# Performance work log

Hardware: AMD Instinct MI355X
Metric: run time of the kernel (lower is better)

The kernel has to match this reference:

```python
import jax, jax.numpy as jnp
import numpy as np

N = 100000   # total nodes in batched graph
E = 320000   # total edges
B = 128      # number of graphs in batch
D_IN = 128
H = 256
OUT = 10
L = 4        # num_layers - 1 conv layers
EPS = 1e-6


def setup_inputs() -> dict:
    key = jax.random.key(0)
    ks = jax.random.split(key, 8)
    h = jax.random.normal(ks[0], (N, D_IN), dtype=jnp.float32)
    src = jax.random.randint(ks[1], (E,), 0, N)
    dst = jax.random.randint(ks[2], (E,), 0, N)
    batch_ids = jnp.sort(jax.random.randint(ks[3], (N,), 0, B))
    s = 0.05
    W_first = jax.random.normal(ks[4], (D_IN, H), dtype=jnp.float32) * s
    b_first = jnp.zeros((H,), jnp.float32)
    W_rest = jax.random.normal(ks[5], (L - 1, H, H), dtype=jnp.float32) * s
    b_rest = jnp.zeros((L - 1, H), jnp.float32)
    gamma = jnp.ones((L, H), jnp.float32)
    beta = jnp.zeros((L, H), jnp.float32)
    mean_scale = jnp.ones((L, H), jnp.float32)
    W_pred = jax.random.normal(ks[6], (H, OUT), dtype=jnp.float32) * s
    b_pred = jnp.zeros((OUT,), jnp.float32)
    return dict(h=h, src=src, dst=dst, batch_ids=batch_ids,
                W_first=W_first, b_first=b_first, W_rest=W_rest, b_rest=b_rest,
                gamma=gamma, beta=beta, mean_scale=mean_scale,
                W_pred=W_pred, b_pred=b_pred)


def _graph_conv(h, W, b, src, dst, dinv_src, dinv_dst):
    # DGL GraphConv, norm='both': D_dst^{-1/2} A D_src^{-1/2} h W + b
    x = h * dinv_src[:, None]
    m = jax.ops.segment_sum(x[src], dst, num_segments=N)
    m = m * dinv_dst[:, None]
    return m @ W + b


def _graph_norm(h, gamma, beta, ms, batch_ids, counts):
    # GraphNorm: per-graph mean (scaled by learnable mean_scale) and std
    mean = jax.ops.segment_sum(h, batch_ids, num_segments=B) / counts[:, None]
    sub = h - mean[batch_ids] * ms
    var = jax.ops.segment_sum(sub * sub, batch_ids, num_segments=B) / counts[:, None]
    inv_std = jax.lax.rsqrt(var + EPS)
    return gamma * sub * inv_std[batch_ids] + beta


def reference(h, src, dst, batch_ids, W_first, b_first, W_rest, b_rest,
              gamma, beta, mean_scale, W_pred, b_pred):
    ones_e = jnp.ones((E,), h.dtype)
    deg_out = jnp.maximum(jax.ops.segment_sum(ones_e, src, num_segments=N), 1.0)
    deg_in = jnp.maximum(jax.ops.segment_sum(ones_e, dst, num_segments=N), 1.0)
    dinv_src = jax.lax.rsqrt(deg_out)
    dinv_dst = jax.lax.rsqrt(deg_in)
    counts = jnp.maximum(
        jax.ops.segment_sum(jnp.ones((N,), h.dtype), batch_ids, num_segments=B), 1.0)

    for i in range(L):
        x = h
        if i == 0:
            h = _graph_conv(h, W_first, b_first, src, dst, dinv_src, dinv_dst)
        else:
            h = _graph_conv(h, W_rest[i - 1], b_rest[i - 1], src, dst, dinv_src, dinv_dst)
        h = _graph_norm(h, gamma[i], beta[i], mean_scale[i], batch_ids, counts)
        if i != 0:
            h = jax.nn.relu(h) + x
        else:
            h = jax.nn.relu(h)

    pooled = jax.ops.segment_sum(h, batch_ids, num_segments=B)  # [B, H]
    # dropout is identity at eval
    return pooled @ W_pred + b_pred
```

## Files before the change

### kernel.cpp

```cpp
#include <hip/hip_runtime.h>

#define N_NODES 100000
#define N_PAD   100096
#define N_EDGES 320000
#define NB      128
#define DIN     128
#define H       256
#define OUT_DIM 10
#define EPSV    1e-6f
#define SCAN_B  256
#define PSLICES 32
#define NBLK    (N_PAD / 64)
#define NXCD    8
#define GEMM_PGRID 1024

typedef unsigned short bf16_t;
typedef __attribute__((ext_vector_type(8))) short bf16x8;
typedef __attribute__((ext_vector_type(4))) float f32x4;

__device__ __forceinline__ float bf2f(bf16_t u) {
    union { unsigned int i; float f; } x;
    x.i = ((unsigned int)u) << 16;
    return x.f;
}
__device__ __forceinline__ bf16_t f2bf(float f) {
    union { float f; unsigned int i; } x;
    x.f = f;
    unsigned int r = x.i + 0x7fffu + ((x.i >> 16) & 1u);
    return (bf16_t)(r >> 16);
}

__device__ __forceinline__ int xcd_swz(int bid, int nwg) {
    int q = nwg / NXCD, r = nwg % NXCD;
    int x = bid % NXCD, j = bid / NXCD;
    int base = (x < r) ? x * (q + 1) : r * (q + 1) + (x - r) * q;
    return base + j;
}

__global__ void k_edge_deg(const int* __restrict__ src, const int* __restrict__ dst,
                           int* deg_out, int* deg_in) {
    int e = blockIdx.x * blockDim.x + threadIdx.x;
    if (e < N_EDGES) {
        atomicAdd(&deg_out[src[e]], 1);
        atomicAdd(&deg_in[dst[e]], 1);
    }
}

__global__ void k_dinv(const int* __restrict__ deg_out, const int* __restrict__ deg_in,
                       float* dinv_src, float* dinv_dst) {
    int n = blockIdx.x * blockDim.x + threadIdx.x;
    if (n < N_NODES) {
        dinv_src[n] = rsqrtf((float)max(deg_out[n], 1));
        dinv_dst[n] = rsqrtf((float)max(deg_in[n], 1));
    }
}

__global__ void k_gstart(const int* __restrict__ bid, int* __restrict__ gstart,
                         float* __restrict__ countsf) {
    int b = threadIdx.x;
    if (b <= NB) {
        int lo = 0, hi = N_NODES;
        while (lo < hi) {
            int mid = (lo + hi) >> 1;
            if (bid[mid] < b) lo = mid + 1; else hi = mid;
        }
        gstart[b] = lo;
    }
    __syncthreads();
    if (b < NB) countsf[b] = (float)max(gstart[b + 1] - gstart[b], 1);
}

__global__ void k_relpk(const int* __restrict__ bid, unsigned int* __restrict__ relpk) {
    int idx = blockIdx.x * blockDim.x + threadIdx.x;
    if (idx >= NBLK * 16) return;
    int t = idx >> 4, w = idx & 15;
    int row0 = t * 64;
    int g0 = bid[(row0 < N_NODES) ? row0 : (N_NODES - 1)];
    unsigned int pk = 0;
    for (int j = 0; j < 4; ++j) {
        int r = row0 + w * 4 + j;
        unsigned int rel = 255u;
        if (r < N_NODES) {
            int d = bid[r] - g0;
            rel = (d >= 0 && d < 255) ? (unsigned int)d : 255u;
        }
        pk |= rel << (8 * j);
    }
    relpk[idx] = pk;
}

__global__ void k_scan1(const int* __restrict__ deg, int* incl, int* bsums) {
    __shared__ int s[SCAN_B];
    int i = blockIdx.x * SCAN_B + threadIdx.x;
    int v = (i < N_NODES) ? deg[i] : 0;
    s[threadIdx.x] = v;
    __syncthreads();
    for (int d = 1; d < SCAN_B; d <<= 1) {
        int t = (threadIdx.x >= d) ? s[threadIdx.x - d] : 0;
        __syncthreads();
        s[threadIdx.x] += t;
        __syncthreads();
    }
    if (i < N_NODES) incl[i] = s[threadIdx.x];
    if (threadIdx.x == SCAN_B - 1) bsums[blockIdx.x] = s[threadIdx.x];
}

__global__ void k_scan2(const int* __restrict__ bsums, int* boffs, int nb) {
    __shared__ int s[512];
    int t = threadIdx.x;
    int v = (t < nb) ? bsums[t] : 0;
    s[t] = v;
    __syncthreads();
    for (int d = 1; d < 512; d <<= 1) {
        int x = (t >= d) ? s[t - d] : 0;
        __syncthreads();
        s[t] += x;
        __syncthreads();
    }
    if (t < nb) boffs[t] = s[t] - v;
}

__global__ void k_scan3(const int* __restrict__ deg, const int* __restrict__ incl,
                        const int* __restrict__ boffs, int* row_start, int* cursor) {
    int i = blockIdx.x * blockDim.x + threadIdx.x;
    if (i < N_NODES) {
        int ex = incl[i] - deg[i] + boffs[i / SCAN_B];
        row_start[i] = ex;
        cursor[i]    = ex;
    }
    if (i == 0) row_start[N_NODES] = N_EDGES;
}

__global__ void k_scatter(const int* __restrict__ src, const int* __restrict__ dst,
                          int* cursor, int* csr_src) {
    int e = blockIdx.x * blockDim.x + threadIdx.x;
    if (e < N_EDGES) {
        int slot = atomicAdd(&cursor[dst[e]], 1);
        csr_src[slot] = src[e];
    }
}

__global__ void k_wt_first(const float* __restrict__ W, bf16_t* __restrict__ Wt) {
    int idx = blockIdx.x * 256 + threadIdx.x;
    if (idx >= H * DIN) return;
    int c = idx / DIN, k = idx % DIN;
    Wt[idx] = f2bf(W[k * H + c]);
}
__global__ void k_wt_rest(const float* __restrict__ W, bf16_t* __restrict__ Wt) {
    int idx = blockIdx.x * 256 + threadIdx.x;
    if (idx >= 3 * H * H) return;
    int l = idx / (H * H);
    int rem = idx % (H * H);
    int c = rem / H, k = rem % H;
    Wt[idx] = f2bf(W[(size_t)l * H * H + k * H + c]);
}

__global__ void k_prescale(const float* __restrict__ h, const float* __restrict__ dinv_s,
                           bf16_t* __restrict__ hs) {
    int idx = xcd_swz(blockIdx.x, 12500) * 256 + threadIdx.x;
    if (idx >= N_NODES * (DIN / 4)) return;
    int n = idx >> 5;
    float w = dinv_s[n];
    float4 v = reinterpret_cast<const float4*>(h)[idx];
    ushort4 o;
    o.x = f2bf(v.x * w); o.y = f2bf(v.y * w);
    o.z = f2bf(v.z * w); o.w = f2bf(v.w * w);
    reinterpret_cast<ushort4*>(hs)[idx] = o;
}

template <int NC, bool PS>
__global__ void k_agg(const bf16_t* __restrict__ hx, const float* __restrict__ dinv_s,
                      const float* __restrict__ dinv_d, const int* __restrict__ row_start,
                      const int* __restrict__ csr_src, bf16_t* __restrict__ m) {
    constexpr int VEC = NC / 64;
    int gid  = xcd_swz(blockIdx.x, 25000) * blockDim.x + threadIdx.x;
    int v    = gid >> 6;
    int lane = gid & 63;
    if (v >= N_NODES) return;
    float acc[VEC] = {};
    int s0 = row_start[v], s1 = row_start[v + 1];

    auto body = [&](int ei) {
        int si = csr_src[ei];
        float wv = 1.f;
        if constexpr (!PS) wv = dinv_s[si];
        if constexpr (VEC == 4) {
            ushort4 r = *reinterpret_cast<const ushort4*>(hx + (size_t)si * NC + lane * 4);
            acc[0] += bf2f(r.x) * wv; acc[1] += bf2f(r.y) * wv;
            acc[2] += bf2f(r.z) * wv; acc[3] += bf2f(r.w) * wv;
        } else {
            ushort2 r = *reinterpret_cast<const ushort2*>(hx + (size_t)si * NC + lane * 2);
            acc[0] += bf2f(r.x) * wv; acc[1] += bf2f(r.y) * wv;
        }
    };

    int e = s0;
    for (; e + 3 < s1; e += 4) { body(e); body(e + 1); body(e + 2); body(e + 3); }
    for (; e < s1; ++e) body(e);

    float wd = dinv_d[v];
    if constexpr (VEC == 4) {
        ushort4 o;
        o.x = f2bf(acc[0] * wd); o.y = f2bf(acc[1] * wd);
        o.z = f2bf(acc[2] * wd); o.w = f2bf(acc[3] * wd);
        *reinterpret_cast<ushort4*>(m + (size_t)v * NC + lane * 4) = o;
    } else {
        ushort2 o; o.x = f2bf(acc[0] * wd); o.y = f2bf(acc[1] * wd);
        *reinterpret_cast<ushort2*>(m + (size_t)v * NC + lane * 2) = o;
    }
}

template <int K>
__global__ __launch_bounds__(256, 2) void k_gemm_mfma(const bf16_t* __restrict__ A,
                                                      const bf16_t* __restrict__ Wt,
                                                      const float* __restrict__ bias,
                                                      const unsigned int* __restrict__ relpk,
                                                      bf16_t* __restrict__ C,
                                                      float2* __restrict__ part) {
    __shared__ bf16_t lds_raw[64 * (H + 8)];
    constexpr int LKA = K + 8;
    bf16_t (*aT)[LKA] = reinterpret_cast<bf16_t (*)[LKA]>(lds_raw);
    bf16_t (*cT)[H + 8] = reinterpret_cast<bf16_t (*)[H + 8]>(lds_raw);
    constexpr int KS = K / 32;

    const int tid  = threadIdx.x;
    const int wave = tid >> 6;
    const int lane = tid & 63;
    const int col0 = wave * 64;
    const int lr = lane & 15;
    const int lg = lane >> 4;

    const bf16_t* Bb = Wt + (size_t)(col0 + lr) * K + lg * 8;
    bf16x8 ball[KS][4];
    #pragma unroll
    for (int ks = 0; ks < KS; ++ks)
        #pragma unroll
        for (int nt = 0; nt < 4; ++nt)
            ball[ks][nt] = *reinterpret_cast<const bf16x8*>(Bb + (size_t)nt * 16 * K + ks * 32);
    float bsn[4];
    #pragma unroll
    for (int nt = 0; nt < 4; ++nt) bsn[nt] = bias[col0 + nt * 16 + lr];

    for (int t = blockIdx.x; t < NBLK; t += GEMM_PGRID) {
        const int pb   = xcd_swz(t, NBLK);
        const int row0 = pb * 64;

        {
            const bf16_t* Ag = A + (size_t)row0 * K;
            constexpr int CHUNKS = 64 * K / 8;
            #pragma unroll
            for (int it = 0; it < CHUNKS / 256; ++it) {
                int ci  = it * 256 + tid;
                int row = (ci * 8) / K;
                int col = (ci * 8) % K;
                uint4 v = *reinterpret_cast<const uint4*>(Ag + ci * 8);
                *reinterpret_cast<uint4*>(&aT[row][col]) = v;
            }
        }
        __syncthreads();

        f32x4 acc[4][4] = {};

        #pragma unroll
        for (int ks = 0; ks < KS; ++ks) {
            bf16x8 a[4];
            #pragma unroll
            for (int mt = 0; mt < 4; ++mt)
                a[mt] = *reinterpret_cast<const bf16x8*>(&aT[mt * 16 + lr][ks * 32 + lg * 8]);
            #pragma unroll
            for (int mt = 0; mt < 4; ++mt)
                #pragma unroll
                for (int nt = 0; nt < 4; ++nt)
                    acc[mt][nt] = __builtin_amdgcn_mfma_f32_16x16x32_bf16(a[mt], ball[ks][nt], acc[mt][nt], 0, 0, 0);
        }

        {
            unsigned int relw[4];
            #pragma unroll
            for (int mt = 0; mt < 4; ++mt)
                relw[mt] = relpk[pb * 16 + mt * 4 + lg];

            float sA[3][4] = {}, qA[3][4] = {};
            #pragma unroll
            for (int mt = 0; mt < 4; ++mt) {
                #pragma unroll
                for (int j = 0; j < 4; ++j) {
                    int rv = (relw[mt] >> (8 * j)) & 0xff;
                    #pragma unroll
                    for (int nt = 0; nt < 4; ++nt) {
                        float v  = acc[mt][nt][j] + bsn[nt];
                        float v0 = (rv == 0) ? v : 0.f;
                        float v1 = (rv == 1) ? v : 0.f;
                        float v2 = (rv == 2) ? v : 0.f;
                        sA[0][nt] += v0; qA[0][nt] += v0 * v0;
                        sA[1][nt] += v1; qA[1][nt] += v1 * v1;
                        sA[2][nt] += v2; qA[2][nt] += v2 * v2;
                    }
                }
            }
            #pragma unroll
            for (int rel = 0; rel < 3; ++rel) {
                #pragma unroll
                for (int nt = 0; nt < 4; ++nt) {
                    float sv = sA[rel][nt], qv = qA[rel][nt];
                    sv += __shfl_xor(sv, 16); qv += __shfl_xor(qv, 16);
                    sv += __shfl_xor(sv, 32); qv += __shfl_xor(qv, 32);
                    sA[rel][nt] = sv; qA[rel][nt] = qv;
                }
            }
            if (lg == 0) {
                constexpr size_t PLANE = (size_t)NBLK * H;
                #pragma unroll
                for (int rel = 0; rel < 3; ++rel)
                    #pragma unroll
                    for (int nt = 0; nt < 4; ++nt)
                        part[(size_t)rel * PLANE + (size_t)pb * H + col0 + nt * 16 + lr]
                            = make_float2(sA[rel][nt], qA[rel][nt]);
            }
        }

        __syncthreads();

        #pragma unroll
        for (int nt = 0; nt < 4; ++nt) {
            int c = col0 + nt * 16 + lr;
            #pragma unroll
            for (int mt = 0; mt < 4; ++mt) {
                #pragma unroll
                for (int j = 0; j < 4; ++j)
                    cT[mt * 16 + lg * 4 + j][c] = f2bf(acc[mt][nt][j] + bsn[nt]);
            }
        }
        __syncthreads();

        #pragma unroll
        for (int it = 0; it < 8; ++it) {
            int i = it * 256 + tid;
            int r = i >> 5;
            int s = i & 31;
            *reinterpret_cast<uint4*>(C + (size_t)(row0 + r) * H + s * 8) =
                *reinterpret_cast<const uint4*>(&cT[r][s * 8]);
        }
        __syncthreads();
    }
}

__global__ void k_stats_red(const float2* __restrict__ part, const int* __restrict__ bid,
                            const int* __restrict__ gstart, const float* __restrict__ countsf,
                            const float* __restrict__ gamma, const float* __restrict__ beta,
                            const float* __restrict__ msc,
                            float* __restrict__ scale, float* __restrict__ shift) {
    constexpr size_t PLANE = (size_t)NBLK * H;
    int b = blockIdx.x;
    int c = threadIdx.x;
    int n0 = gstart[b], n1 = gstart[b + 1];
    float s = 0.f, q = 0.f;
    if (n1 > n0) {
        int blo = n0 >> 6, bhi = (n1 - 1) >> 6;
        for (int blk = blo; blk <= bhi; ++blk) {
            int rel = b - bid[blk << 6];
            if (rel >= 0 && rel < 3) {
                float2 v = part[(size_t)rel * PLANE + (size_t)blk * H + c];
                s += v.x; q += v.y;
            }
        }
    }
    float rc   = 1.0f / countsf[b];
    float mean = s * rc, ex2 = q * rc;
    float mm   = mean * msc[c];
    float var  = ex2 - 2.f * mean * mm + mm * mm;
    float a    = gamma[c] * rsqrtf(var + EPSV);
    scale[b * H + c] = a;
    shift[b * H + c] = beta[c] - a * mm;
}

template <bool RES>
__global__ void k_norm(const bf16_t* __restrict__ y, const bf16_t* __restrict__ resid,
                       const int* __restrict__ bid, const float* __restrict__ scale,
                       const float* __restrict__ shift, bf16_t* __restrict__ outp) {
    int idx = xcd_swz(blockIdx.x, 25000) * 256 + threadIdx.x;
    if (idx >= N_NODES * (H / 4)) return;
    int n  = idx >> 6;
    int f4 = idx & 63;
    int b  = bid[n];
    float4 sc = reinterpret_cast<const float4*>(scale)[b * 64 + f4];
    float4 sh = reinterpret_cast<const float4*>(shift)[b * 64 + f4];
    ushort4 yv = reinterpret_cast<const ushort4*>(y)[idx];
    float o0 = fmaxf(bf2f(yv.x) * sc.x + sh.x, 0.f);
    float o1 = fmaxf(bf2f(yv.y) * sc.y + sh.y, 0.f);
    float o2 = fmaxf(bf2f(yv.z) * sc.z + sh.z, 0.f);
    float o3 = fmaxf(bf2f(yv.w) * sc.w + sh.w, 0.f);
    if constexpr (RES) {
        ushort4 r = reinterpret_cast<const ushort4*>(resid)[idx];
        o0 += bf2f(r.x); o1 += bf2f(r.y); o2 += bf2f(r.z); o3 += bf2f(r.w);
    }
    ushort4 o;
    o.x = f2bf(o0); o.y = f2bf(o1); o.z = f2bf(o2); o.w = f2bf(o3);
    reinterpret_cast<ushort4*>(outp)[idx] = o;
}

__global__ void k_pool(const bf16_t* __restrict__ hf, const int* __restrict__ gstart,
                       float* pooled) {
    int b = blockIdx.x, sl = blockIdx.y, f = threadIdx.x;
    int n0 = gstart[b], n1 = gstart[b + 1];
    int cnt = n1 - n0;
    int lo = n0 + (int)((long long)cnt * sl / PSLICES);
    int hi = n0 + (int)((long long)cnt * (sl + 1) / PSLICES);
    if (lo >= hi) return;
    float s = 0.f;
    for (int n = lo; n < hi; ++n) s += bf2f(hf[(size_t)n * H + f]);
    atomicAdd(&pooled[b * H + f], s);
}

__global__ void k_pred(const float* __restrict__ pooled, const float* __restrict__ Wp,
                       const float* __restrict__ bp, float* __restrict__ outp) {
    __shared__ float row[H];
    int b = blockIdx.x;
    row[threadIdx.x] = pooled[b * H + threadIdx.x];
    __syncthreads();
    if (threadIdx.x < OUT_DIM) {
        float acc = bp[threadIdx.x];
        for (int f = 0; f < H; ++f) acc += row[f] * Wp[f * OUT_DIM + threadIdx.x];
        outp[b * OUT_DIM + threadIdx.x] = acc;
    }
}

extern "C" void kernel_launch(void* const* d_in, const int* in_sizes, int n_in,
                              void* d_out, int out_size, void* d_ws, size_t ws_size,
                              hipStream_t stream) {
    const float* h_in  = (const float*)d_in[0];
    const int*   src   = (const int*)d_in[1];
    const int*   dst   = (const int*)d_in[2];
    const int*   bid   = (const int*)d_in[3];
    const float* Wf    = (const float*)d_in[4];
    const float* bfv   = (const float*)d_in[5];
    const float* Wr    = (const float*)d_in[6];
    const float* br    = (const float*)d_in[7];
    const float* gamma = (const float*)d_in[8];
    const float* beta  = (const float*)d_in[9];
    const float* ms    = (const float*)d_in[10];
    const float* Wp    = (const float*)d_in[11];
    const float* bp    = (const float*)d_in[12];
    float* outp = (float*)d_out;

    char* w = (char*)d_ws;
    size_t off = 0;
    auto alloc = [&](size_t bytes) -> void* {
        void* p = w + off;
        off = (off + bytes + 255) & ~(size_t)255;
        return p;
    };
    bf16_t* bufA = (bf16_t*)alloc((size_t)N_PAD * H * 2);
    bf16_t* bufB = (bf16_t*)alloc((size_t)N_PAD * H * 2);
    bf16_t* bufC = (bf16_t*)alloc((size_t)N_PAD * H * 2);
    bf16_t* Wt0  = (bf16_t*)alloc((size_t)H * DIN * 2);
    bf16_t* Wt123= (bf16_t*)alloc((size_t)3 * H * H * 2);
    int* deg_out_i = (int*)alloc(N_NODES * 4);
    int* deg_in_i  = (int*)alloc(N_NODES * 4);
    float* dinv_src = (float*)alloc(N_NODES * 4);
    float* dinv_dst = (float*)alloc(N_NODES * 4);
    int* incl_tmp  = (int*)alloc(N_NODES * 4);
    int* bsums     = (int*)alloc(512 * 4);
    int* boffs     = (int*)alloc(512 * 4);
    int* row_start = (int*)alloc((N_NODES + 1) * 4);
    int* cursor    = (int*)alloc(N_NODES * 4);
    int* csr_src   = (int*)alloc(N_EDGES * 4);
    int* gstart    = (int*)alloc((NB + 1) * 4);
    float* countsf = (float*)alloc(NB * 4);
    float* gscale  = (float*)alloc((size_t)NB * H * 4);
    float* gshift  = (float*)alloc((size_t)NB * H * 4);
    float2* part   = (float2*)alloc((size_t)3 * NBLK * H * 8);
    unsigned int* relpk = (unsigned int*)alloc((size_t)NBLK * 16 * 4);
    float* pooled  = (float*)alloc(NB * H * 4);

    if (off > ws_size) return;

    bf16_t* hs = bufB;

    const int nscan = (N_NODES + SCAN_B - 1) / SCAN_B;

    hipMemsetAsync(deg_out_i, 0, N_NODES * 4, stream);
    hipMemsetAsync(deg_in_i, 0, N_NODES * 4, stream);
    hipMemsetAsync(pooled, 0, NB * H * 4, stream);

    k_edge_deg<<<(N_EDGES + 255) / 256, 256, 0, stream>>>(src, dst, deg_out_i, deg_in_i);
    k_gstart<<<1, 256, 0, stream>>>(bid, gstart, countsf);
    k_relpk<<<(NBLK * 16 + 255) / 256, 256, 0, stream>>>(bid, relpk);
    k_dinv<<<(N_NODES + 255) / 256, 256, 0, stream>>>(deg_out_i, deg_in_i, dinv_src, dinv_dst);
    k_scan1<<<nscan, SCAN_B, 0, stream>>>(deg_in_i, incl_tmp, bsums);
    k_scan2<<<1, 512, 0, stream>>>(bsums, boffs, nscan);
    k_scan3<<<(N_NODES + 255) / 256, 256, 0, stream>>>(deg_in_i, incl_tmp, boffs, row_start, cursor);
    k_scatter<<<(N_EDGES + 255) / 256, 256, 0, stream>>>(src, dst, cursor, csr_src);
    k_wt_first<<<(H * DIN + 255) / 256, 256, 0, stream>>>(Wf, Wt0);
    k_wt_rest<<<(3 * H * H + 255) / 256, 256, 0, stream>>>(Wr, Wt123);

    const int aggGrid  = (N_NODES + 3) / 4;
    const int normGrid = (N_NODES * (H / 4) + 255) / 256;

    k_prescale<<<(N_NODES * (DIN / 4) + 255) / 256, 256, 0, stream>>>(h_in, dinv_src, hs);
    k_agg<DIN, true><<<aggGrid, 256, 0, stream>>>(hs, nullptr, dinv_dst, row_start, csr_src, bufA);
    k_gemm_mfma<DIN><<<GEMM_PGRID, 256, 0, stream>>>(bufA, Wt0, bfv, relpk, bufB, part);
    k_stats_red<<<NB, H, 0, stream>>>(part, bid, gstart, countsf, gamma, beta, ms,
                                      gscale, gshift);
    k_norm<false><<<normGrid, 256, 0, stream>>>(bufB, nullptr, bid, gscale, gshift, bufC);

    bf16_t* hx = bufC;
    bf16_t* f1 = bufA;
    bf16_t* f2 = bufB;
    for (int i = 1; i < 4; ++i) {
        k_agg<H, false><<<aggGrid, 256, 0, stream>>>(hx, dinv_src, dinv_dst, row_start, csr_src, f1);
        k_gemm_mfma<H><<<GEMM_PGRID, 256, 0, stream>>>(f1, Wt123 + (size_t)(i - 1) * H * H,
                                                       br + (i - 1) * H, relpk, f2, part);
        k_stats_red<<<NB, H, 0, stream>>>(part, bid, gstart, countsf, gamma + i * H,
                                          beta + i * H, ms + i * H, gscale, gshift);
        k_norm<true><<<normGrid, 256, 0, stream>>>(f2, hx, bid, gscale, gshift, f1);
        bf16_t* nh = f1; f1 = hx; hx = nh;
    }

    k_pool<<<dim3(NB, PSLICES), H, 0, stream>>>(hx, gstart, pooled);
    k_pred<<<NB, H, 0, stream>>>(pooled, Wp, bp, outp);
}
```

Baseline: 630.8 us.

## Merge setup kernels, drop memsets, and launch one GEMM block per row tile

Merges several small setup kernels into fewer launches: degree counting into one buffer, gstart with relpk, dinv computed in scan3, and the two weight-transpose kernels into one. Two of the three memsets are gone. Pooling now writes per-slice partials that k_pred reduces, instead of using atomics on a zeroed buffer. The GEMM drops its persistent grid-stride loop and launches one block per 64-row tile, which removes the loop-carried syncs but reloads the B weights into registers in every block.

```diff
diff --git a/kernel.cpp b/kernel.cpp
--- a/kernel.cpp
+++ b/kernel.cpp
@@ -12,7 +12,6 @@
 #define PSLICES 32
 #define NBLK    (N_PAD / 64)
 #define NXCD    8
-#define GEMM_PGRID 1024
 
 typedef unsigned short bf16_t;
 typedef __attribute__((ext_vector_type(8))) short bf16x8;
@@ -38,39 +37,29 @@
 }
 
 __global__ void k_edge_deg(const int* __restrict__ src, const int* __restrict__ dst,
-                           int* deg_out, int* deg_in) {
+                           int* deg) {
     int e = blockIdx.x * blockDim.x + threadIdx.x;
     if (e < N_EDGES) {
-        atomicAdd(&deg_out[src[e]], 1);
-        atomicAdd(&deg_in[dst[e]], 1);
-    }
-}
-
-__global__ void k_dinv(const int* __restrict__ deg_out, const int* __restrict__ deg_in,
-                       float* dinv_src, float* dinv_dst) {
-    int n = blockIdx.x * blockDim.x + threadIdx.x;
-    if (n < N_NODES) {
-        dinv_src[n] = rsqrtf((float)max(deg_out[n], 1));
-        dinv_dst[n] = rsqrtf((float)max(deg_in[n], 1));
-    }
-}
-
-__global__ void k_gstart(const int* __restrict__ bid, int* __restrict__ gstart,
-                         float* __restrict__ countsf) {
-    int b = threadIdx.x;
-    if (b <= NB) {
-        int lo = 0, hi = N_NODES;
-        while (lo < hi) {
-            int mid = (lo + hi) >> 1;
-            if (bid[mid] < b) lo = mid + 1; else hi = mid;
-        }
-        gstart[b] = lo;
-    }
-    __syncthreads();
-    if (b < NB) countsf[b] = (float)max(gstart[b + 1] - gstart[b], 1);
-}
-
-__global__ void k_relpk(const int* __restrict__ bid, unsigned int* __restrict__ relpk) {
+        atomicAdd(&deg[src[e]], 1);
+        atomicAdd(&deg[N_NODES + dst[e]], 1);
+    }
+}
+
+__global__ void k_gstart_relpk(const int* __restrict__ bid, int* __restrict__ gstart,
+                               float* __restrict__ countsf, unsigned int* __restrict__ relpk) {
+    if (blockIdx.x == 0) {
+        int b = threadIdx.x;
+        if (b <= NB) {
+            int lo = 0, hi = N_NODES;
+            while (lo < hi) {
+                int mid = (lo + hi) >> 1;
+                if (bid[mid] < b) lo = mid + 1; else hi = mid;
+            }
+            gstart[b] = lo;
+        }
+        __syncthreads();
+        if (b < NB) countsf[b] = (float)max(gstart[b + 1] - gstart[b], 1);
+    }
     int idx = blockIdx.x * blockDim.x + threadIdx.x;
     if (idx >= NBLK * 16) return;
     int t = idx >> 4, w = idx & 15;
@@ -89,10 +78,10 @@
     relpk[idx] = pk;
 }
 
-__global__ void k_scan1(const int* __restrict__ deg, int* incl, int* bsums) {
+__global__ void k_scan1(const int* __restrict__ deg_in, int* incl, int* bsums) {
     __shared__ int s[SCAN_B];
     int i = blockIdx.x * SCAN_B + threadIdx.x;
-    int v = (i < N_NODES) ? deg[i] : 0;
+    int v = (i < N_NODES) ? deg_in[i] : 0;
     s[threadIdx.x] = v;
     __syncthreads();
     for (int d = 1; d < SCAN_B; d <<= 1) {
@@ -121,12 +110,15 @@
 }
 
 __global__ void k_scan3(const int* __restrict__ deg, const int* __restrict__ incl,
-                        const int* __restrict__ boffs, int* row_start, int* cursor) {
+                        const int* __restrict__ boffs, int* row_start, int* cursor,
+                        float* dinv_src, float* dinv_dst) {
     int i = blockIdx.x * blockDim.x + threadIdx.x;
     if (i < N_NODES) {
-        int ex = incl[i] - deg[i] + boffs[i / SCAN_B];
+        int ex = incl[i] - deg[N_NODES + i] + boffs[i / SCAN_B];
         row_start[i] = ex;
         cursor[i]    = ex;
+        dinv_src[i] = rsqrtf((float)max(deg[i], 1));
+        dinv_dst[i] = rsqrtf((float)max(deg[N_NODES + i], 1));
     }
     if (i == 0) row_start[N_NODES] = N_EDGES;
 }
@@ -140,19 +132,20 @@
     }
 }
 
-__global__ void k_wt_first(const float* __restrict__ W, bf16_t* __restrict__ Wt) {
+__global__ void k_wt(const float* __restrict__ Wf, const float* __restrict__ Wr,
+                     bf16_t* __restrict__ Wt0, bf16_t* __restrict__ Wt123) {
     int idx = blockIdx.x * 256 + threadIdx.x;
-    if (idx >= H * DIN) return;
-    int c = idx / DIN, k = idx % DIN;
-    Wt[idx] = f2bf(W[k * H + c]);
-}
-__global__ void k_wt_rest(const float* __restrict__ W, bf16_t* __restrict__ Wt) {
-    int idx = blockIdx.x * 256 + threadIdx.x;
+    if (idx < H * DIN) {
+        int c = idx / DIN, k = idx % DIN;
+        Wt0[idx] = f2bf(Wf[k * H + c]);
+        return;
+    }
+    idx -= H * DIN;
     if (idx >= 3 * H * H) return;
     int l = idx / (H * H);
     int rem = idx % (H * H);
     int c = rem / H, k = rem % H;
-    Wt[idx] = f2bf(W[(size_t)l * H * H + k * H + c]);
+    Wt123[idx] = f2bf(Wr[(size_t)l * H * H + k * H + c]);
 }
 
 __global__ void k_prescale(const float* __restrict__ h, const float* __restrict__ dinv_s,
@@ -226,6 +219,8 @@
     const int tid  = threadIdx.x;
     const int wave = tid >> 6;
     const int lane = tid & 63;
+    const int pb   = xcd_swz(blockIdx.x, NBLK);
+    const int row0 = pb * 64;
     const int col0 = wave * 64;
     const int lr = lane & 15;
     const int lg = lane >> 4;
@@ -237,111 +232,106 @@
         #pragma unroll
         for (int nt = 0; nt < 4; ++nt)
             ball[ks][nt] = *reinterpret_cast<const bf16x8*>(Bb + (size_t)nt * 16 * K + ks * 32);
+
+    {
+        const bf16_t* Ag = A + (size_t)row0 * K;
+        constexpr int CHUNKS = 64 * K / 8;
+        #pragma unroll
+        for (int it = 0; it < CHUNKS / 256; ++it) {
+            int ci  = it * 256 + tid;
+            int row = (ci * 8) / K;
+            int col = (ci * 8) % K;
+            uint4 v = *reinterpret_cast<const uint4*>(Ag + ci * 8);
+            *reinterpret_cast<uint4*>(&aT[row][col]) = v;
+        }
+    }
+    __syncthreads();
+
+    f32x4 acc[4][4] = {};
+
+    #pragma unroll
+    for (int ks = 0; ks < KS; ++ks) {
+        bf16x8 a[4];
+        #pragma unroll
+        for (int mt = 0; mt < 4; ++mt)
+            a[mt] = *reinterpret_cast<const bf16x8*>(&aT[mt * 16 + lr][ks * 32 + lg * 8]);
+        #pragma unroll
+        for (int mt = 0; mt < 4; ++mt)
+            #pragma unroll
+            for (int nt = 0; nt < 4; ++nt)
+                acc[mt][nt] = __builtin_amdgcn_mfma_f32_16x16x32_bf16(a[mt], ball[ks][nt], acc[mt][nt], 0, 0, 0);
+    }
+
     float bsn[4];
     #pragma unroll
     for (int nt = 0; nt < 4; ++nt) bsn[nt] = bias[col0 + nt * 16 + lr];
 
-    for (int t = blockIdx.x; t < NBLK; t += GEMM_PGRID) {
-        const int pb   = xcd_swz(t, NBLK);
-        const int row0 = pb * 64;
-
-        {
-            const bf16_t* Ag = A + (size_t)row0 * K;
-            constexpr int CHUNKS = 64 * K / 8;
+    {
+        unsigned int relw[4];
+        #pragma unroll
+        for (int mt = 0; mt < 4; ++mt)
+            relw[mt] = relpk[pb * 16 + mt * 4 + lg];
+
+        float sA[3][4] = {}, qA[3][4] = {};
+        #pragma unroll
+        for (int mt = 0; mt < 4; ++mt) {
             #pragma unroll
-            for (int it = 0; it < CHUNKS / 256; ++it) {
-                int ci  = it * 256 + tid;
-                int row = (ci * 8) / K;
-                int col = (ci * 8) % K;
-                uint4 v = *reinterpret_cast<const uint4*>(Ag + ci * 8);
-                *reinterpret_cast<uint4*>(&aT[row][col]) = v;
+            for (int j = 0; j < 4; ++j) {
+                int rv = (relw[mt] >> (8 * j)) & 0xff;
+                #pragma unroll
+                for (int nt = 0; nt < 4; ++nt) {
+                    float v  = acc[mt][nt][j] + bsn[nt];
+                    float v0 = (rv == 0) ? v : 0.f;
+                    float v1 = (rv == 1) ? v : 0.f;
+                    float v2 = (rv == 2) ? v : 0.f;
+                    sA[0][nt] += v0; qA[0][nt] += v0 * v0;
+                    sA[1][nt] += v1; qA[1][nt] += v1 * v1;
+                    sA[2][nt] += v2; qA[2][nt] += v2 * v2;
+                }
             }
         }
-        __syncthreads();
-
-        f32x4 acc[4][4] = {};
-
-        #pragma unroll
-        for (int ks = 0; ks < KS; ++ks) {
-            bf16x8 a[4];
+        #pragma unroll
+        for (int rel = 0; rel < 3; ++rel) {
             #pragma unroll
-            for (int mt = 0; mt < 4; ++mt)
-                a[mt] = *reinterpret_cast<const bf16x8*>(&aT[mt * 16 + lr][ks * 32 + lg * 8]);
+            for (int nt = 0; nt < 4; ++nt) {
+                float sv = sA[rel][nt], qv = qA[rel][nt];
+                sv += __shfl_xor(sv, 16); qv += __shfl_xor(qv, 16);
+                sv += __shfl_xor(sv, 32); qv += __shfl_xor(qv, 32);
+                sA[rel][nt] = sv; qA[rel][nt] = qv;
+            }
+        }
+        if (lg == 0) {
+            constexpr size_t PLANE = (size_t)NBLK * H;
             #pragma unroll
-            for (int mt = 0; mt < 4; ++mt)
+            for (int rel = 0; rel < 3; ++rel)
                 #pragma unroll
                 for (int nt = 0; nt < 4; ++nt)
-                    acc[mt][nt] = __builtin_amdgcn_mfma_f32_16x16x32_bf16(a[mt], ball[ks][nt], acc[mt][nt], 0, 0, 0);
-        }
-
-        {
-            unsigned int relw[4];
+                    part[(size_t)rel * PLANE + (size_t)pb * H + col0 + nt * 16 + lr]
+                        = make_float2(sA[rel][nt], qA[rel][nt]);
+        }
+    }
+
+    __syncthreads();
+
+    #pragma unroll
+    for (int nt = 0; nt < 4; ++nt) {
+        int c = col0 + nt * 16 + lr;
+        #pragma unroll
+        for (int mt = 0; mt < 4; ++mt) {
             #pragma unroll
-            for (int mt = 0; mt < 4; ++mt)
-                relw[mt] = relpk[pb * 16 + mt * 4 + lg];
-
-            float sA[3][4] = {}, qA[3][4] = {};
-            #pragma unroll
-            for (int mt = 0; mt < 4; ++mt) {
-                #pragma unroll
-                for (int j = 0; j < 4; ++j) {
-                    int rv = (relw[mt] >> (8 * j)) & 0xff;
-                    #pragma unroll
-                    for (int nt = 0; nt < 4; ++nt) {
-                        float v  = acc[mt][nt][j] + bsn[nt];
-                        float v0 = (rv == 0) ? v : 0.f;
-                        float v1 = (rv == 1) ? v : 0.f;
-                        float v2 = (rv == 2) ? v : 0.f;
-                        sA[0][nt] += v0; qA[0][nt] += v0 * v0;
-                        sA[1][nt] += v1; qA[1][nt] += v1 * v1;
-                        sA[2][nt] += v2; qA[2][nt] += v2 * v2;
-                    }
-                }
-            }
-            #pragma unroll
-            for (int rel = 0; rel < 3; ++rel) {
-                #pragma unroll
-                for (int nt = 0; nt < 4; ++nt) {
-                    float sv = sA[rel][nt], qv = qA[rel][nt];
-                    sv += __shfl_xor(sv, 16); qv += __shfl_xor(qv, 16);
-                    sv += __shfl_xor(sv, 32); qv += __shfl_xor(qv, 32);
-                    sA[rel][nt] = sv; qA[rel][nt] = qv;
-                }
-            }
-            if (lg == 0) {
-                constexpr size_t PLANE = (size_t)NBLK * H;
-                #pragma unroll
-                for (int rel = 0; rel < 3; ++rel)
-                    #pragma unroll
-                    for (int nt = 0; nt < 4; ++nt)
-                        part[(size_t)rel * PLANE + (size_t)pb * H + col0 + nt * 16 + lr]
-                            = make_float2(sA[rel][nt], qA[rel][nt]);
-            }
-        }
-
-        __syncthreads();
-
-        #pragma unroll
-        for (int nt = 0; nt < 4; ++nt) {
-            int c = col0 + nt * 16 + lr;
-            #pragma unroll
-            for (int mt = 0; mt < 4; ++mt) {
-                #pragma unroll
-                for (int j = 0; j < 4; ++j)
-                    cT[mt * 16 + lg * 4 + j][c] = f2bf(acc[mt][nt][j] + bsn[nt]);
-            }
-        }
-        __syncthreads();
-
-        #pragma unroll
-        for (int it = 0; it < 8; ++it) {
-            int i = it * 256 + tid;
-            int r = i >> 5;
-            int s = i & 31;
-            *reinterpret_cast<uint4*>(C + (size_t)(row0 + r) * H + s * 8) =
-                *reinterpret_cast<const uint4*>(&cT[r][s * 8]);
-        }
-        __syncthreads();
+            for (int j = 0; j < 4; ++j)
+                cT[mt * 16 + lg * 4 + j][c] = f2bf(acc[mt][nt][j] + bsn[nt]);
+        }
+    }
+    __syncthreads();
+
+    #pragma unroll
+    for (int it = 0; it < 8; ++it) {
+        int i = it * 256 + tid;
+        int r = i >> 5;
+        int s = i & 31;
+        *reinterpret_cast<uint4*>(C + (size_t)(row0 + r) * H + s * 8) =
+            *reinterpret_cast<const uint4*>(&cT[r][s * 8]);
     }
 }
 
@@ -400,28 +390,30 @@
 }
 
 __global__ void k_pool(const bf16_t* __restrict__ hf, const int* __restrict__ gstart,
-                       float* pooled) {
+                       float* __restrict__ pp) {
     int b = blockIdx.x, sl = blockIdx.y, f = threadIdx.x;
     int n0 = gstart[b], n1 = gstart[b + 1];
     int cnt = n1 - n0;
     int lo = n0 + (int)((long long)cnt * sl / PSLICES);
     int hi = n0 + (int)((long long)cnt * (sl + 1) / PSLICES);
-    if (lo >= hi) return;
     float s = 0.f;
     for (int n = lo; n < hi; ++n) s += bf2f(hf[(size_t)n * H + f]);
-    atomicAdd(&pooled[b * H + f], s);
-}
-
-__global__ void k_pred(const float* __restrict__ pooled, const float* __restrict__ Wp,
+    pp[((size_t)b * PSLICES + sl) * H + f] = s;
+}
+
+__global__ void k_pred(const float* __restrict__ pp, const float* __restrict__ Wp,
                        const float* __restrict__ bp, float* __restrict__ outp) {
     __shared__ float row[H];
-    int b = blockIdx.x;
-    row[threadIdx.x] = pooled[b * H + threadIdx.x];
+    int b = blockIdx.x, f = threadIdx.x;
+    float s = 0.f;
+    for (int sl = 0; sl < PSLICES; ++sl)
+        s += pp[((size_t)b * PSLICES + sl) * H + f];
+    row[f] = s;
     __syncthreads();
-    if (threadIdx.x < OUT_DIM) {
-        float acc = bp[threadIdx.x];
-        for (int f = 0; f < H; ++f) acc += row[f] * Wp[f * OUT_DIM + threadIdx.x];
-        outp[b * OUT_DIM + threadIdx.x] = acc;
+    if (f < OUT_DIM) {
+        float acc = bp[f];
+        for (int k = 0; k < H; ++k) acc += row[k] * Wp[k * OUT_DIM + f];
+        outp[b * OUT_DIM + f] = acc;
     }
 }
 
@@ -455,8 +447,7 @@
     bf16_t* bufC = (bf16_t*)alloc((size_t)N_PAD * H * 2);
     bf16_t* Wt0  = (bf16_t*)alloc((size_t)H * DIN * 2);
     bf16_t* Wt123= (bf16_t*)alloc((size_t)3 * H * H * 2);
-    int* deg_out_i = (int*)alloc(N_NODES * 4);
-    int* deg_in_i  = (int*)alloc(N_NODES * 4);
+    int* deg       = (int*)alloc((size_t)2 * N_NODES * 4);
     float* dinv_src = (float*)alloc(N_NODES * 4);
     float* dinv_dst = (float*)alloc(N_NODES * 4);
     int* incl_tmp  = (int*)alloc(N_NODES * 4);
@@ -471,7 +462,7 @@
     float* gshift  = (float*)alloc((size_t)NB * H * 4);
     float2* part   = (float2*)alloc((size_t)3 * NBLK * H * 8);
     unsigned int* relpk = (unsigned int*)alloc((size_t)NBLK * 16 * 4);
-    float* pooled  = (float*)alloc(NB * H * 4);
+    float* pp      = (float*)alloc((size_t)NB * PSLICES * H * 4);
 
     if (off > ws_size) return;
 
@@ -479,27 +470,23 @@
 
     const int nscan = (N_NODES + SCAN_B - 1) / SCAN_B;
 
-    hipMemsetAsync(deg_out_i, 0, N_NODES * 4, stream);
-    hipMemsetAsync(deg_in_i, 0, N_NODES * 4, stream);
-    hipMemsetAsync(pooled, 0, NB * H * 4, stream);
-
-    k_edge_deg<<<(N_EDGES + 255) / 256, 256, 0, stream>>>(src, dst, deg_out_i, deg_in_i);
-    k_gstart<<<1, 256, 0, stream>>>(bid, gstart, countsf);
-    k_relpk<<<(NBLK * 16 + 255) / 256, 256, 0, stream>>>(bid, relpk);
-    k_dinv<<<(N_NODES + 255) / 256, 256, 0, stream>>>(deg_out_i, deg_in_i, dinv_src, dinv_dst);
-    k_scan1<<<nscan, SCAN_B, 0, stream>>>(deg_in_i, incl_tmp, bsums);
+    hipMemsetAsync(deg, 0, (size_t)2 * N_NODES * 4, stream);
+
+    k_edge_deg<<<(N_EDGES + 255) / 256, 256, 0, stream>>>(src, dst, deg);
+    k_gstart_relpk<<<(NBLK * 16 + 255) / 256, 256, 0, stream>>>(bid, gstart, countsf, relpk);
+    k_scan1<<<nscan, SCAN_B, 0, stream>>>(deg + N_NODES, incl_tmp, bsums);
     k_scan2<<<1, 512, 0, stream>>>(bsums, boffs, nscan);
-    k_scan3<<<(N_NODES + 255) / 256, 256, 0, stream>>>(deg_in_i, incl_tmp, boffs, row_start, cursor);
+    k_scan3<<<(N_NODES + 255) / 256, 256, 0, stream>>>(deg, incl_tmp, boffs, row_start, cursor,
+                                                       dinv_src, dinv_dst);
     k_scatter<<<(N_EDGES + 255) / 256, 256, 0, stream>>>(src, dst, cursor, csr_src);
-    k_wt_first<<<(H * DIN + 255) / 256, 256, 0, stream>>>(Wf, Wt0);
-    k_wt_rest<<<(3 * H * H + 255) / 256, 256, 0, stream>>>(Wr, Wt123);
+    k_wt<<<(H * DIN + 3 * H * H + 255) / 256, 256, 0, stream>>>(Wf, Wr, Wt0, Wt123);
 
     const int aggGrid  = (N_NODES + 3) / 4;
     const int normGrid = (N_NODES * (H / 4) + 255) / 256;
 
     k_prescale<<<(N_NODES * (DIN / 4) + 255) / 256, 256, 0, stream>>>(h_in, dinv_src, hs);
     k_agg<DIN, true><<<aggGrid, 256, 0, stream>>>(hs, nullptr, dinv_dst, row_start, csr_src, bufA);
-    k_gemm_mfma<DIN><<<GEMM_PGRID, 256, 0, stream>>>(bufA, Wt0, bfv, relpk, bufB, part);
+    k_gemm_mfma<DIN><<<NBLK, 256, 0, stream>>>(bufA, Wt0, bfv, relpk, bufB, part);
     k_stats_red<<<NB, H, 0, stream>>>(part, bid, gstart, countsf, gamma, beta, ms,
                                       gscale, gshift);
     k_norm<false><<<normGrid, 256, 0, stream>>>(bufB, nullptr, bid, gscale, gshift, bufC);
@@ -509,14 +496,14 @@
     bf16_t* f2 = bufB;
     for (int i = 1; i < 4; ++i) {
         k_agg<H, false><<<aggGrid, 256, 0, stream>>>(hx, dinv_src, dinv_dst, row_start, csr_src, f1);
-        k_gemm_mfma<H><<<GEMM_PGRID, 256, 0, stream>>>(f1, Wt123 + (size_t)(i - 1) * H * H,
-                                                       br + (i - 1) * H, relpk, f2, part);
+        k_gemm_mfma<H><<<NBLK, 256, 0, stream>>>(f1, Wt123 + (size_t)(i - 1) * H * H,
+                                                 br + (i - 1) * H, relpk, f2, part);
         k_stats_red<<<NB, H, 0, stream>>>(part, bid, gstart, countsf, gamma + i * H,
                                           beta + i * H, ms + i * H, gscale, gshift);
         k_norm<true><<<normGrid, 256, 0, stream>>>(f2, hx, bid, gscale, gshift, f1);
         bf16_t* nh = f1; f1 = hx; hx = nh;
     }
 
-    k_pool<<<dim3(NB, PSLICES), H, 0, stream>>>(hx, gstart, pooled);
-    k_pred<<<NB, H, 0, stream>>>(pooled, Wp, bp, outp);
-}
+    k_pool<<<dim3(NB, PSLICES), H, 0, stream>>>(hx, gstart, pp);
+    k_pred<<<NB, H, 0, stream>>>(pp, Wp, bp, outp);
+}
```

Measured after the change: 561.4 us (median of 2 runs). -11.0%, faster.
